# Kernel tuning notes

Hardware: AMD Instinct MI355X
Metric: run time of the kernel (lower is better)

The kernel has to match this reference:

```python
import jax, jax.numpy as jnp
import numpy as np

B, T, D, K = 16, 4096, 256, 1024

def setup_inputs() -> dict:
    key = jax.random.key(0)
    k1, k2 = jax.random.split(key)
    inputs = jax.random.normal(k1, (B, T, D), dtype=jnp.float32)
    codebook = jax.random.normal(k2, (K, D), dtype=jnp.float32)
    return {"inputs": inputs, "codebook": codebook}

def reference(inputs, codebook):
    # argmin over squared distance == argmin over L2 distance (cdist p=2).
    x2 = jnp.sum(inputs * inputs, axis=-1, keepdims=True)          # [B,T,1]
    c2 = jnp.sum(codebook * codebook, axis=-1)                      # [K]
    xc = jnp.einsum('btd,kd->btk', inputs, codebook)                # [B,T,K]
    d2 = x2 + c2[None, None, :] - 2.0 * xc                          # [B,T,K]
    assignment = jnp.argmin(d2, axis=-1)                            # [B,T]
    quantized = codebook[assignment]                                # [B,T,D]
    # Straight-through estimator
    out = jax.lax.stop_gradient(quantized - inputs) + inputs
    return out
```

## Files before the change

kernel.cpp:

```cpp
#include <hip/hip_runtime.h>
#include <float.h>


typedef _Float16 f16;
typedef f16 f16x8 __attribute__((ext_vector_type(8)));
typedef f16 f16x4 __attribute__((ext_vector_type(4)));
typedef float f32x4 __attribute__((ext_vector_type(4)));

#define DDIM    256
#define KCODES  1024
#define NTOK    65536
#define SMARGIN 0.1f

__global__ __launch_bounds__(256) void vq_prep(const float* __restrict__ cb,
                                               f16* __restrict__ cht,
                                               float* __restrict__ c2,
                                               unsigned* __restrict__ count) {
    const int k    = blockIdx.x * 4 + (threadIdx.x >> 6);
    const int lane = threadIdx.x & 63;
    const float4 v = *(const float4*)(cb + (size_t)k * DDIM + 4 * lane);
    f16x4 h; h[0] = (f16)v.x; h[1] = (f16)v.y; h[2] = (f16)v.z; h[3] = (f16)v.w;
    const int ct = k >> 4, m = k & 15;
    const int e  = 4 * lane;
    const int kt = e >> 5;
    const int s  = (e & 31) >> 3;
    const int j0 = e & 7;
    const int L  = s * 16 + m;
    *(f16x4*)(cht + ((size_t)(ct * 8 + kt) * 64 + L) * 8 + j0) = h;
    float ssum = v.x * v.x + v.y * v.y + v.z * v.z + v.w * v.w;
    #pragma unroll
    for (int off = 32; off > 0; off >>= 1) ssum += __shfl_down(ssum, off, 64);
    if (lane == 0) c2[k] = ssum;
    if (blockIdx.x == 0 && threadIdx.x == 0) *count = 0u;
}

#define SLICE(CUR, S, NPTR, NS) do {                                                \
    _Pragma("unroll")                                                               \
    for (int ci = 0; ci < 4; ++ci)                                                  \
        _Pragma("unroll")                                                           \
        for (int ti = 0; ti < 4; ++ti)                                              \
            acc[ci][ti] = __builtin_amdgcn_mfma_f32_16x16x32_f16(                   \
                CUR[ci], bfrag[ti][S], acc[ci][ti], 0, 0, 0);                       \
    _Pragma("unroll")                                                               \
    for (int ci = 0; ci < 4; ++ci)                                                  \
        CUR[ci] = *(const f16x8*)((NPTR) + ci * 4096 + (NS) * 512);                 \
} while (0)

__global__ __launch_bounds__(256, 2) void vq_main(const float* __restrict__ xg,
                                                  const f16* __restrict__ cht,
                                                  const float* __restrict__ c2,
                                                  const float* __restrict__ cb,
                                                  float* __restrict__ out,
                                                  unsigned* __restrict__ count,
                                                  unsigned* __restrict__ list) {
    __shared__ float c2s[KCODES];
    __shared__ float wmv[2][128];
    __shared__ int   wmi[2][128];
    __shared__ float wms[2][128];
    __shared__ int   idx_s[128];

    const int t    = threadIdx.x;
    const int wave = t >> 6, lane = t & 63;
    const int wm   = wave >> 1;
    const int tn   = wave & 1;
    const int q    = lane >> 4;
    const int m16  = lane & 15;
    const int tok0 = blockIdx.x * 128;

    *(float4*)&c2s[t * 4] = *(const float4*)(c2 + t * 4);
    __syncthreads();

    const f16* aw = cht + wm * 16384 + lane * 8;

    f16x8 afA[4], afB[4];
    #pragma unroll
    for (int ci = 0; ci < 4; ++ci) afA[ci] = *(const f16x8*)(aw + ci * 4096 + 0 * 512);
    #pragma unroll
    for (int ci = 0; ci < 4; ++ci) afB[ci] = *(const f16x8*)(aw + ci * 4096 + 1 * 512);

    f16x8 bfrag[4][8];
    #pragma unroll
    for (int ti = 0; ti < 4; ++ti) {
        const size_t row = (size_t)(tok0 + tn * 64 + ti * 16 + m16) * DDIM;
        #pragma unroll
        for (int ks = 0; ks < 8; ++ks) {
            const float* p = xg + row + ks * 32 + q * 8;
            const float4 u0 = *(const float4*)(p);
            const float4 u1 = *(const float4*)(p + 4);
            f16x8 b;
            b[0] = (f16)u0.x; b[1] = (f16)u0.y; b[2] = (f16)u0.z; b[3] = (f16)u0.w;
            b[4] = (f16)u1.x; b[5] = (f16)u1.y; b[6] = (f16)u1.z; b[7] = (f16)u1.w;
            bfrag[ti][ks] = b;
        }
    }

    float rb1[4], rb2[4]; int ri1[4];
    #pragma unroll
    for (int ti = 0; ti < 4; ++ti) { rb1[ti] = -FLT_MAX; rb2[ti] = -FLT_MAX; ri1[ti] = 0; }

    #pragma unroll 1
    for (int nc = 0; nc < 8; ++nc) {
        f32x4 acc[4][4];
        #pragma unroll
        for (int ci = 0; ci < 4; ++ci) {
            f32x4 cv = *(const f32x4*)&c2s[nc * 128 + wm * 64 + ci * 16 + q * 4];
            cv = cv * -0.5f;
            #pragma unroll
            for (int ti = 0; ti < 4; ++ti) acc[ci][ti] = cv;
        }

        const f16* an = aw + nc * 32768;
        const f16* ax = aw + ((nc + 1) & 7) * 32768;

        __builtin_amdgcn_s_setprio(1);
        SLICE(afA, 0, an, 2);
        SLICE(afB, 1, an, 3);
        SLICE(afA, 2, an, 4);
        SLICE(afB, 3, an, 5);
        SLICE(afA, 4, an, 6);
        SLICE(afB, 5, an, 7);
        SLICE(afA, 6, ax, 0);
        SLICE(afB, 7, ax, 1);
        __builtin_amdgcn_s_setprio(0);

        const int kbase = nc * 128 + wm * 64;
        #pragma unroll
        for (int ti = 0; ti < 4; ++ti) {
            float b1 = -FLT_MAX, b2 = -FLT_MAX; int i1 = 0;
            #pragma unroll
            for (int ci = 0; ci < 4; ++ci) {
                #pragma unroll
                for (int r = 0; r < 4; ++r) {
                    const float v = acc[ci][ti][r];
                    const int   c = kbase + ci * 16 + q * 4 + r;
                    const bool gt = v > b1;
                    b2 = fmaxf(b2, gt ? b1 : v);
                    i1 = gt ? c : i1;
                    b1 = gt ? v : b1;
                }
            }
            #pragma unroll
            for (int sft = 0; sft < 2; ++sft) {
                const int off = 16 << sft;
                const float ob1 = __shfl_xor(b1, off, 64);
                const float ob2 = __shfl_xor(b2, off, 64);
                const int   oi1 = __shfl_xor(i1, off, 64);
                const bool better = (ob1 > b1) || (ob1 == b1 && oi1 < i1);
                b2 = fmaxf(fmaxf(b2, ob2), fminf(b1, ob1));
                b1 = better ? ob1 : b1;
                i1 = better ? oi1 : i1;
            }
            rb2[ti] = fmaxf(fmaxf(rb2[ti], b2), fminf(rb1[ti], b1));
            if (b1 > rb1[ti]) { rb1[ti] = b1; ri1[ti] = i1; }
        }
    }

    #pragma unroll
    for (int ti = 0; ti < 4; ++ti) {
        if (lane < 16) {
            const int tl = tn * 64 + ti * 16 + m16;
            wmv[wm][tl] = rb1[ti]; wmi[wm][tl] = ri1[ti]; wms[wm][tl] = rb2[ti];
        }
    }
    __syncthreads();
    if (t < 128) {
        const float a1 = wmv[0][t], a2 = wms[0][t];
        const int   ai = wmi[0][t];
        const float b1_ = wmv[1][t], b2_ = wms[1][t];
        const int   bi_ = wmi[1][t];
        const bool bb = (b1_ > a1) || (b1_ == a1 && bi_ < ai);
        const float c1 = bb ? b1_ : a1;
        const int   ci_ = bb ? bi_ : ai;
        const float cs = fmaxf(fmaxf(a2, b2_), fminf(a1, b1_));
        idx_s[t] = ci_;
        if (c1 - cs < SMARGIN) {
            const unsigned p = atomicAdd(count, 1u);
            list[p] = tok0 + t;
        }
    }
    __syncthreads();

    #pragma unroll
    for (int i = 0; i < 32; ++i) {
        const int f   = i * 256 + t;
        const int tok = f >> 6, d4 = f & 63;
        const int code = idx_s[tok];
        const float4 v = *(const float4*)(cb + (size_t)code * DDIM + 4 * d4);
        *(float4*)(out + (size_t)(tok0 + tok) * DDIM + 4 * d4) = v;
    }
}

__global__ __launch_bounds__(256) void vq_rescue(const float* __restrict__ xg,
                                                 const float* __restrict__ cb,
                                                 const float* __restrict__ c2,
                                                 const unsigned* __restrict__ count,
                                                 const unsigned* __restrict__ list,
                                                 float* __restrict__ out) {
    __shared__ float xls[8][DDIM];
    __shared__ float rv[4][8];
    __shared__ int   ri[4][8];
    __shared__ int   bidx[8];

    const int t = threadIdx.x;
    const int wave = t >> 6, lane = t & 63;
    const unsigned n = *count;

    for (unsigned base = blockIdx.x * 8; base < n; base += gridDim.x * 8) {
        const int nb = (int)min(8u, n - base);
        __syncthreads();
        #pragma unroll
        for (int i = 0; i < 2; ++i) {
            const int f = t + 256 * i;
            const int row = f >> 6, d4 = f & 63;
            if (row < nb)
                *(float4*)&xls[row][4 * d4] =
                    *(const float4*)(xg + (size_t)list[base + row] * DDIM + 4 * d4);
        }
        __syncthreads();

        float acc[4][8];
        #pragma unroll
        for (int j = 0; j < 4; ++j)
            #pragma unroll
            for (int tk = 0; tk < 8; ++tk) acc[j][tk] = 0.0f;

        for (int d4 = 0; d4 < 64; ++d4) {
            float4 cv[4];
            #pragma unroll
            for (int j = 0; j < 4; ++j)
                cv[j] = *(const float4*)(cb + (size_t)(4 * t + j) * DDIM + 4 * d4);
            #pragma unroll
            for (int tk = 0; tk < 8; ++tk) {
                const float4 xv = *(const float4*)&xls[tk][4 * d4];
                #pragma unroll
                for (int j = 0; j < 4; ++j) {
                    float a = acc[j][tk];
                    a = fmaf(cv[j].x, xv.x, a);
                    a = fmaf(cv[j].y, xv.y, a);
                    a = fmaf(cv[j].z, xv.z, a);
                    a = fmaf(cv[j].w, xv.w, a);
                    acc[j][tk] = a;
                }
            }
        }

        #pragma unroll
        for (int tk = 0; tk < 8; ++tk) {
            if (tk < nb) {
                float b1 = FLT_MAX; int i1 = 0;
                #pragma unroll
                for (int j = 0; j < 4; ++j) {
                    const float d = fmaf(-2.0f, acc[j][tk], c2[4 * t + j]);
                    if (d < b1) { b1 = d; i1 = 4 * t + j; }
                }
                #pragma unroll
                for (int off = 32; off > 0; off >>= 1) {
                    const float ov = __shfl_xor(b1, off, 64);
                    const int   oi = __shfl_xor(i1, off, 64);
                    if (ov < b1 || (ov == b1 && oi < i1)) { b1 = ov; i1 = oi; }
                }
                if (lane == 0) { rv[wave][tk] = b1; ri[wave][tk] = i1; }
            }
        }
        __syncthreads();
        if (t < 8 && t < nb) {
            float bv = rv[0][t]; int bi = ri[0][t];
            #pragma unroll
            for (int w = 1; w < 4; ++w)
                if (rv[w][t] < bv || (rv[w][t] == bv && ri[w][t] < bi)) {
                    bv = rv[w][t]; bi = ri[w][t];
                }
            bidx[t] = bi;
        }
        __syncthreads();

        #pragma unroll
        for (int i = 0; i < 2; ++i) {
            const int f = t + 256 * i;
            const int row = f >> 6, d4 = f & 63;
            if (row < nb) {
                const int code = bidx[row];
                const float4 v = *(const float4*)(cb + (size_t)code * DDIM + 4 * d4);
                *(float4*)(out + (size_t)list[base + row] * DDIM + 4 * d4) = v;
            }
        }
    }
}

extern "C" void kernel_launch(void* const* d_in, const int* in_sizes, int n_in,
                              void* d_out, int out_size, void* d_ws, size_t ws_size,
                              hipStream_t stream) {
    const float* x  = (const float*)d_in[0];
    const float* cb = (const float*)d_in[1];
    float* out = (float*)d_out;

    char* ws = (char*)d_ws;
    f16*      cht   = (f16*)ws;
    float*    c2    = (float*)(ws + 524288);
    unsigned* count = (unsigned*)(ws + 528448);
    unsigned* list  = (unsigned*)(ws + 528512);

    hipLaunchKernelGGL(vq_prep,   dim3(KCODES / 4), dim3(256), 0, stream, cb, cht, c2, count);
    hipLaunchKernelGGL(vq_main,   dim3(NTOK / 128), dim3(256), 0, stream,
                       x, cht, c2, cb, out, count, list);
    hipLaunchKernelGGL(vq_rescue, dim3(1024),       dim3(256), 0, stream,
                       x, cb, c2, count, list, out);
}
```

Measured before the change: 228.5 us.

## Halve token tile, raise occupancy, and pack code index into score mantissa bits

Shrinks each block's token tile from 128 to 64 so every wave holds half the B fragments and accumulators, and raises launch bounds to three blocks per CU. The inner argmin loop drops its per-chunk index tracking and shuffle reduction. Instead it embeds a 7-bit local code index in the low mantissa bits of each score and keeps running max and second-max with plain fmax/fmin. The cross-lane shuffle merge now runs once at the end instead of once per codebook chunk. The trade-off is twice as many blocks, each re-streaming the full codebook, with less codebook reuse per token, plus slight score perturbation that the margin-based rescue pass must absorb.

```diff
diff --git a/kernel.cpp b/kernel.cpp
--- a/kernel.cpp
+++ b/kernel.cpp
@@ -10,6 +10,7 @@
 #define DDIM    256
 #define KCODES  1024
 #define NTOK    65536
+#define TOKB    64
 #define SMARGIN 0.1f
 
 __global__ __launch_bounds__(256) void vq_prep(const float* __restrict__ cb,
@@ -38,7 +39,7 @@
     _Pragma("unroll")                                                               \
     for (int ci = 0; ci < 4; ++ci)                                                  \
         _Pragma("unroll")                                                           \
-        for (int ti = 0; ti < 4; ++ti)                                              \
+        for (int ti = 0; ti < 2; ++ti)                                              \
             acc[ci][ti] = __builtin_amdgcn_mfma_f32_16x16x32_f16(                   \
                 CUR[ci], bfrag[ti][S], acc[ci][ti], 0, 0, 0);                       \
     _Pragma("unroll")                                                               \
@@ -46,7 +47,7 @@
         CUR[ci] = *(const f16x8*)((NPTR) + ci * 4096 + (NS) * 512);                 \
 } while (0)
 
-__global__ __launch_bounds__(256, 2) void vq_main(const float* __restrict__ xg,
+__global__ __launch_bounds__(256, 3) void vq_main(const float* __restrict__ xg,
                                                   const f16* __restrict__ cht,
                                                   const float* __restrict__ c2,
                                                   const float* __restrict__ cb,
@@ -54,10 +55,10 @@
                                                   unsigned* __restrict__ count,
                                                   unsigned* __restrict__ list) {
     __shared__ float c2s[KCODES];
-    __shared__ float wmv[2][128];
-    __shared__ int   wmi[2][128];
-    __shared__ float wms[2][128];
-    __shared__ int   idx_s[128];
+    __shared__ float wmv[2][TOKB];
+    __shared__ int   wmi[2][TOKB];
+    __shared__ float wms[2][TOKB];
+    __shared__ int   idx_s[TOKB];
 
     const int t    = threadIdx.x;
     const int wave = t >> 6, lane = t & 63;
@@ -65,7 +66,7 @@
     const int tn   = wave & 1;
     const int q    = lane >> 4;
     const int m16  = lane & 15;
-    const int tok0 = blockIdx.x * 128;
+    const int tok0 = blockIdx.x * TOKB;
 
     *(float4*)&c2s[t * 4] = *(const float4*)(c2 + t * 4);
     __syncthreads();
@@ -78,10 +79,10 @@
     #pragma unroll
     for (int ci = 0; ci < 4; ++ci) afB[ci] = *(const f16x8*)(aw + ci * 4096 + 1 * 512);
 
-    f16x8 bfrag[4][8];
-    #pragma unroll
-    for (int ti = 0; ti < 4; ++ti) {
-        const size_t row = (size_t)(tok0 + tn * 64 + ti * 16 + m16) * DDIM;
+    f16x8 bfrag[2][8];
+    #pragma unroll
+    for (int ti = 0; ti < 2; ++ti) {
+        const size_t row = (size_t)(tok0 + tn * 32 + ti * 16 + m16) * DDIM;
         #pragma unroll
         for (int ks = 0; ks < 8; ++ks) {
             const float* p = xg + row + ks * 32 + q * 8;
@@ -94,19 +95,19 @@
         }
     }
 
-    float rb1[4], rb2[4]; int ri1[4];
-    #pragma unroll
-    for (int ti = 0; ti < 4; ++ti) { rb1[ti] = -FLT_MAX; rb2[ti] = -FLT_MAX; ri1[ti] = 0; }
+    float rb1[2], rb2[2];
+    #pragma unroll
+    for (int ti = 0; ti < 2; ++ti) { rb1[ti] = -FLT_MAX; rb2[ti] = -FLT_MAX; }
 
     #pragma unroll 1
     for (int nc = 0; nc < 8; ++nc) {
-        f32x4 acc[4][4];
+        f32x4 acc[4][2];
         #pragma unroll
         for (int ci = 0; ci < 4; ++ci) {
             f32x4 cv = *(const f32x4*)&c2s[nc * 128 + wm * 64 + ci * 16 + q * 4];
             cv = cv * -0.5f;
             #pragma unroll
-            for (int ti = 0; ti < 4; ++ti) acc[ci][ti] = cv;
+            for (int ti = 0; ti < 2; ++ti) acc[ci][ti] = cv;
         }
 
         const f16* an = aw + nc * 32768;
@@ -123,47 +124,46 @@
         SLICE(afB, 7, ax, 1);
         __builtin_amdgcn_s_setprio(0);
 
-        const int kbase = nc * 128 + wm * 64;
-        #pragma unroll
-        for (int ti = 0; ti < 4; ++ti) {
-            float b1 = -FLT_MAX, b2 = -FLT_MAX; int i1 = 0;
+        #pragma unroll
+        for (int ti = 0; ti < 2; ++ti) {
             #pragma unroll
             for (int ci = 0; ci < 4; ++ci) {
                 #pragma unroll
                 for (int r = 0; r < 4; ++r) {
-                    const float v = acc[ci][ti][r];
-                    const int   c = kbase + ci * 16 + q * 4 + r;
-                    const bool gt = v > b1;
-                    b2 = fmaxf(b2, gt ? b1 : v);
-                    i1 = gt ? c : i1;
-                    b1 = gt ? v : b1;
+                    const unsigned pv = (__float_as_uint(acc[ci][ti][r]) & ~127u)
+                                        | (unsigned)(127 - (nc * 16 + ci * 4 + r));
+                    const float pf = __uint_as_float(pv);
+                    rb2[ti] = fmaxf(rb2[ti], fminf(rb1[ti], pf));
+                    rb1[ti] = fmaxf(rb1[ti], pf);
                 }
             }
-            #pragma unroll
-            for (int sft = 0; sft < 2; ++sft) {
-                const int off = 16 << sft;
-                const float ob1 = __shfl_xor(b1, off, 64);
-                const float ob2 = __shfl_xor(b2, off, 64);
-                const int   oi1 = __shfl_xor(i1, off, 64);
-                const bool better = (ob1 > b1) || (ob1 == b1 && oi1 < i1);
-                b2 = fmaxf(fmaxf(b2, ob2), fminf(b1, ob1));
-                b1 = better ? ob1 : b1;
-                i1 = better ? oi1 : i1;
-            }
-            rb2[ti] = fmaxf(fmaxf(rb2[ti], b2), fminf(rb1[ti], b1));
-            if (b1 > rb1[ti]) { rb1[ti] = b1; ri1[ti] = i1; }
-        }
-    }
-
-    #pragma unroll
-    for (int ti = 0; ti < 4; ++ti) {
+        }
+    }
+
+    #pragma unroll
+    for (int ti = 0; ti < 2; ++ti) {
+        const int jj = 127 - (int)(__float_as_uint(rb1[ti]) & 127u);
+        int   i1 = (jj >> 4) * 128 + wm * 64 + ((jj >> 2) & 3) * 16 + q * 4 + (jj & 3);
+        float b1 = rb1[ti], b2 = rb2[ti];
+        #pragma unroll
+        for (int sft = 0; sft < 2; ++sft) {
+            const int off = 16 << sft;
+            const float ob1 = __shfl_xor(b1, off, 64);
+            const float ob2 = __shfl_xor(b2, off, 64);
+            const int   oi1 = __shfl_xor(i1, off, 64);
+            const bool better = (ob1 > b1) || (ob1 == b1 && oi1 < i1);
+            b2 = fmaxf(fmaxf(b2, ob2), fminf(b1, ob1));
+            b1 = better ? ob1 : b1;
+            i1 = better ? oi1 : i1;
+        }
         if (lane < 16) {
-            const int tl = tn * 64 + ti * 16 + m16;
-            wmv[wm][tl] = rb1[ti]; wmi[wm][tl] = ri1[ti]; wms[wm][tl] = rb2[ti];
+            const int tl = tn * 32 + ti * 16 + m16;
+            wmv[wm][tl] = b1; wmi[wm][tl] = i1; wms[wm][tl] = b2;
         }
     }
     __syncthreads();
-    if (t < 128) {
+
+    if (t < TOKB) {
         const float a1 = wmv[0][t], a2 = wms[0][t];
         const int   ai = wmi[0][t];
         const float b1_ = wmv[1][t], b2_ = wms[1][t];
@@ -181,7 +181,7 @@
     __syncthreads();
 
     #pragma unroll
-    for (int i = 0; i < 32; ++i) {
+    for (int i = 0; i < 16; ++i) {
         const int f   = i * 256 + t;
         const int tok = f >> 6, d4 = f & 63;
         const int code = idx_s[tok];
@@ -301,7 +301,7 @@
     unsigned* list  = (unsigned*)(ws + 528512);
 
     hipLaunchKernelGGL(vq_prep,   dim3(KCODES / 4), dim3(256), 0, stream, cb, cht, c2, count);
-    hipLaunchKernelGGL(vq_main,   dim3(NTOK / 128), dim3(256), 0, stream,
+    hipLaunchKernelGGL(vq_main,   dim3(NTOK / TOKB), dim3(256), 0, stream,
                        x, cht, c2, cb, out, count, list);
     hipLaunchKernelGGL(vq_rescue, dim3(1024),       dim3(256), 0, stream,
                        x, cb, c2, count, list, out);
```

Result: slower. 240.7 us (+5.3%).
